# Kernel tuning notes

Measured on AMD Instinct MI355X. Metric: run time of the kernel, lower is better.

Reference implementation:

```python
import jax, jax.numpy as jnp
import numpy as np

NUM_EXPERTS = 8
TOP_K = 2

def setup_inputs() -> dict:
    key = jax.random.key(0)
    ks = jax.random.split(key, 5)
    B, S, D, F, E = 4, 2048, 1024, 4096, NUM_EXPERTS
    x = jax.random.normal(ks[0], (B, S, D), dtype=jnp.float32)
    router_w = jax.random.normal(ks[1], (D, E), dtype=jnp.float32) * 0.02
    router_b = jnp.zeros((E,), dtype=jnp.float32)
    w1 = jax.random.normal(ks[2], (E, D, F), dtype=jnp.float32) * 0.02
    b1 = jnp.zeros((E, F), dtype=jnp.float32)
    w2 = jax.random.normal(ks[3], (E, F, D), dtype=jnp.float32) * 0.02
    b2 = jnp.zeros((E, D), dtype=jnp.float32)
    return {"x": x, "router_w": router_w, "router_b": router_b,
            "w1": w1, "b1": b1, "w2": w2, "b2": b2}

def reference(x, router_w, router_b, w1, b1, w2, b2):
    B, S, D = x.shape
    E = router_w.shape[1]
    x_flat = x.reshape(-1, D)                                  # [N, D]
    router_probs = jax.nn.softmax(x_flat @ router_w + router_b, axis=-1)  # [N, E]
    topk_probs, topk_idx = jax.lax.top_k(router_probs, TOP_K)  # [N, K]
    topk_probs = topk_probs / jnp.sum(topk_probs, axis=-1, keepdims=True)
    # combine weight per (token, expert): sum over top-k slots assigned to that expert
    cw = jnp.sum(topk_probs[..., None] * jax.nn.one_hot(topk_idx, E, dtype=x.dtype), axis=1)  # [N, E]
    out = jnp.zeros_like(x_flat)
    for e in range(E):  # small fixed expert count; each iter is a dense GEMM pair
        h = jax.nn.gelu(x_flat @ w1[e] + b1[e], approximate=False)  # [N, F]
        out = out + cw[:, e:e + 1] * (h @ w2[e] + b2[e])            # [N, D]
    return out.reshape(B, S, D)
```

## Files before the change

### kernel.cpp

```cpp
#include <hip/hip_runtime.h>
#include <hip/hip_bf16.h>

typedef __attribute__((ext_vector_type(8))) __bf16 bf16x8;
typedef __attribute__((ext_vector_type(4))) float f32x4;

#define NTOK 8192
#define D_DIM 1024
#define F_DIM 4096
#define NEXP 8
#define SLOT_TOT 16384
#define SLOT_CAP 16512

__device__ __forceinline__ unsigned short f2b(float f) {
  __hip_bfloat16 b = __float2bfloat16(f);
  return reinterpret_cast<unsigned short&>(b);
}

__device__ __forceinline__ void gload_lds16(const void* g, void* l) {
  __builtin_amdgcn_global_load_lds(
      (__attribute__((address_space(1))) void*)g,
      (__attribute__((address_space(3))) void*)l, 16, 0, 0);
}


__global__ void init_counts_kernel(int* counts) {
  if (threadIdx.x < NEXP) counts[threadIdx.x] = 0;
}

__global__ void zero_out_kernel(float* out) {
  const int i = blockIdx.x * 256 + threadIdx.x;
  reinterpret_cast<float4*>(out)[i] = make_float4(0.f, 0.f, 0.f, 0.f);
}

__global__ void convert_x_kernel(const float* __restrict__ x,
                                 __hip_bfloat16* __restrict__ xb) {
  const int i = (blockIdx.x * 256 + threadIdx.x) * 4;
  const float4 v = *reinterpret_cast<const float4*>(x + i);
  union { unsigned short u[4]; uint2 d; } o;
  o.u[0] = f2b(v.x); o.u[1] = f2b(v.y); o.u[2] = f2b(v.z); o.u[3] = f2b(v.w);
  *reinterpret_cast<uint2*>(xb + i) = o.d;
}

__global__ void transpose_conv_kernel(const float* __restrict__ src,
                                      __hip_bfloat16* __restrict__ dst,
                                      int R, int C) {
  __shared__ float tile[32][33];
  const int e = blockIdx.z;
  src += (size_t)e * R * C;
  dst += (size_t)e * R * C;
  const int c0 = blockIdx.x * 32, r0 = blockIdx.y * 32;
  const int tx = threadIdx.x, ty = threadIdx.y;
  #pragma unroll
  for (int j = 0; j < 32; j += 8)
    tile[ty + j][tx] = src[(size_t)(r0 + ty + j) * C + c0 + tx];
  __syncthreads();
  #pragma unroll
  for (int j = 0; j < 32; j += 8)
    dst[(size_t)(c0 + ty + j) * R + r0 + tx] = __float2bfloat16(tile[tx][ty + j]);
}

__global__ void router_kernel(const float* __restrict__ x,
                              const float* __restrict__ rw,
                              const float* __restrict__ rb,
                              int* __restrict__ topk_idx,
                              float* __restrict__ topk_w,
                              int* __restrict__ counts) {
  __shared__ float rwT[NEXP * D_DIM];
  const int tid = threadIdx.x;
  for (int i = tid; i < NEXP * D_DIM; i += 256) {
    const int d = i >> 3, e = i & 7;
    rwT[e * D_DIM + d] = rw[i];
  }
  __syncthreads();

  const int wave = tid >> 6, lane = tid & 63;
  const int tok = blockIdx.x * 4 + wave;
  const float* xr = x + (size_t)tok * D_DIM;

  float acc[NEXP];
  #pragma unroll
  for (int e = 0; e < NEXP; ++e) acc[e] = 0.f;

  for (int i = 0; i < D_DIM / 64; ++i) {
    const int d = i * 64 + lane;
    const float xv = xr[d];
    #pragma unroll
    for (int e = 0; e < NEXP; ++e) acc[e] += xv * rwT[e * D_DIM + d];
  }
  #pragma unroll
  for (int off = 32; off > 0; off >>= 1) {
    #pragma unroll
    for (int e = 0; e < NEXP; ++e) acc[e] += __shfl_xor(acc[e], off);
  }

  if (lane == 0) {
    float l[NEXP];
    #pragma unroll
    for (int e = 0; e < NEXP; ++e) l[e] = acc[e] + rb[e];
    int i1 = 0;
    #pragma unroll
    for (int e = 1; e < NEXP; ++e) if (l[e] > l[i1]) i1 = e;
    int i2 = (i1 == 0) ? 1 : 0;
    #pragma unroll
    for (int e = 0; e < NEXP; ++e) if (e != i1 && e != i2 && l[e] > l[i2]) i2 = e;
    const float w1 = 1.f / (1.f + __expf(l[i2] - l[i1]));
    topk_idx[tok * 2 + 0] = i1;
    topk_idx[tok * 2 + 1] = i2;
    topk_w[tok * 2 + 0] = w1;
    topk_w[tok * 2 + 1] = 1.f - w1;
    atomicAdd(&counts[i1], 1);
    atomicAdd(&counts[i2], 1);
  }
}

__global__ void offsets_kernel(const int* __restrict__ counts,
                               int* __restrict__ offsets,
                               int* __restrict__ cursors,
                               int* __restrict__ slot_token,
                               float* __restrict__ slot_cw) {
  const int t = threadIdx.x;
  if (t == 0) {
    int s = 0;
    for (int e = 0; e < NEXP; ++e) { offsets[e] = s; cursors[e] = s; s += counts[e]; }
    offsets[NEXP] = s;
  }
  if (t < SLOT_CAP - SLOT_TOT) {
    slot_token[SLOT_TOT + t] = 0;
    slot_cw[SLOT_TOT + t] = 0.f;
  }
}

__global__ void scatter_kernel(const int* __restrict__ topk_idx,
                               const float* __restrict__ topk_w,
                               int* __restrict__ cursors,
                               int* __restrict__ slot_token,
                               float* __restrict__ slot_cw) {
  const int tok = blockIdx.x * 256 + threadIdx.x;
  if (tok >= NTOK) return;
  #pragma unroll
  for (int k = 0; k < 2; ++k) {
    const int e = topk_idx[tok * 2 + k];
    const int p = atomicAdd(&cursors[e], 1);
    slot_token[p] = tok;
    slot_cw[p] = topk_w[tok * 2 + k];
  }
}

template <int PHASE>
__global__ __launch_bounds__(256, 2) void moe_gemm(
    const __hip_bfloat16* __restrict__ A,
    const __hip_bfloat16* __restrict__ B,
    const float* __restrict__ bias,
    const int* __restrict__ slot_token,
    const float* __restrict__ slot_cw,
    const int* __restrict__ counts,
    const int* __restrict__ offsets,
    __hip_bfloat16* __restrict__ Hout,
    float* __restrict__ Out) {
  constexpr int K = (PHASE == 1) ? D_DIM : F_DIM;
  constexpr int NCOL = (PHASE == 1) ? F_DIM : D_DIM;

  const int e = blockIdx.z;
  const int cnt = counts[e];
  const int mt = blockIdx.y;
  if (mt * 128 >= cnt) return;
  const int nt = blockIdx.x;
  const int base = offsets[e];

  __shared__ unsigned short lA[4096];
  __shared__ unsigned short lB[4096];

  const int tid = threadIdx.x;
  const int w = tid >> 6, lane = tid & 63;
  const int r = lane & 15, kg = lane >> 4;
  const int wm = w >> 1, wn = w & 1;

  const int rowA0 = mt * 128 + w * 16 + r;
  const int rowA1 = mt * 128 + (4 + w) * 16 + r;
  const __hip_bfloat16 *gA0, *gA1;
  if constexpr (PHASE == 1) {
    gA0 = A + (size_t)slot_token[base + rowA0] * K + kg * 8;
    gA1 = A + (size_t)slot_token[base + rowA1] * K + kg * 8;
  } else {
    gA0 = A + (size_t)(base + rowA0) * K + kg * 8;
    gA1 = A + (size_t)(base + rowA1) * K + kg * 8;
  }
  const __hip_bfloat16* Be = B + (size_t)e * NCOL * K;
  const __hip_bfloat16* gB0 = Be + (size_t)(nt * 128 + w * 16 + r) * K + kg * 8;
  const __hip_bfloat16* gB1 = Be + (size_t)(nt * 128 + (4 + w) * 16 + r) * K + kg * 8;

  unsigned short* lA0 = &lA[w * 512];
  unsigned short* lA1 = &lA[(4 + w) * 512];
  unsigned short* lB0 = &lB[w * 512];
  unsigned short* lB1 = &lB[(4 + w) * 512];

  f32x4 acc[4][4] = {};

  for (int kt = 0; kt < K / 32; ++kt) {
    gload_lds16(gA0, lA0);
    gload_lds16(gA1, lA1);
    gload_lds16(gB0, lB0);
    gload_lds16(gB1, lB1);
    gA0 += 32; gA1 += 32; gB0 += 32; gB1 += 32;
    __syncthreads();

    bf16x8 af[4], bfr[4];
    #pragma unroll
    for (int i = 0; i < 4; ++i) {
      af[i]  = *(const bf16x8*)&lA[(wm * 4 + i) * 512 + lane * 8];
      bfr[i] = *(const bf16x8*)&lB[(wn * 4 + i) * 512 + lane * 8];
    }
    #pragma unroll
    for (int mi = 0; mi < 4; ++mi)
      #pragma unroll
      for (int ni = 0; ni < 4; ++ni)
        acc[mi][ni] = __builtin_amdgcn_mfma_f32_16x16x32_bf16(af[mi], bfr[ni], acc[mi][ni], 0, 0, 0);
    __syncthreads();
  }

  const int rem = cnt - mt * 128;
  const int q4 = (lane >> 4) * 4;

  if constexpr (PHASE == 1) {
    #pragma unroll
    for (int ni = 0; ni < 4; ++ni) {
      const int col = nt * 128 + wn * 64 + ni * 16 + (lane & 15);
      const float bv = bias[e * NCOL + col];
      #pragma unroll
      for (int mi = 0; mi < 4; ++mi) {
        #pragma unroll
        for (int rr = 0; rr < 4; ++rr) {
          const int rloc = wm * 64 + mi * 16 + q4 + rr;
          if (rloc < rem) {
            float v = acc[mi][ni][rr] + bv;
            v = 0.5f * v * (1.f + erff(v * 0.70710678118654752f));
            Hout[(size_t)(base + mt * 128 + rloc) * F_DIM + col] = __float2bfloat16(v);
          }
        }
      }
    }
  } else {
    #pragma unroll
    for (int mi = 0; mi < 4; ++mi) {
      int toks[4]; float cws[4];
      #pragma unroll
      for (int rr = 0; rr < 4; ++rr) {
        const int rloc = wm * 64 + mi * 16 + q4 + rr;
        const int slot = base + mt * 128 + rloc;
        const bool ok = (rloc < rem);
        toks[rr] = ok ? slot_token[slot] : -1;
        cws[rr]  = ok ? slot_cw[slot] : 0.f;
      }
      #pragma unroll
      for (int ni = 0; ni < 4; ++ni) {
        const int col = nt * 128 + wn * 64 + ni * 16 + (lane & 15);
        const float bv = bias[e * NCOL + col];
        #pragma unroll
        for (int rr = 0; rr < 4; ++rr) {
          if (toks[rr] >= 0)
            atomicAdd(&Out[(size_t)toks[rr] * D_DIM + col], cws[rr] * (acc[mi][ni][rr] + bv));
        }
      }
    }
  }
}


extern "C" void kernel_launch(void* const* d_in, const int* in_sizes, int n_in,
                              void* d_out, int out_size, void* d_ws, size_t ws_size,
                              hipStream_t stream) {
  const float* x  = (const float*)d_in[0];
  const float* rw = (const float*)d_in[1];
  const float* rb = (const float*)d_in[2];
  const float* w1 = (const float*)d_in[3];
  const float* b1 = (const float*)d_in[4];
  const float* w2 = (const float*)d_in[5];
  const float* b2 = (const float*)d_in[6];
  float* out = (float*)d_out;

  char* p = (char*)d_ws;
  size_t used = 0;
  auto carve = [&](size_t bytes) {
    char* r = p + used;
    used += (bytes + 255) & ~(size_t)255;
    return (void*)r;
  };
  __hip_bfloat16* xb  = (__hip_bfloat16*)carve((size_t)NTOK * D_DIM * 2);
  __hip_bfloat16* w1t = (__hip_bfloat16*)carve((size_t)NEXP * F_DIM * D_DIM * 2);
  __hip_bfloat16* w2t = (__hip_bfloat16*)carve((size_t)NEXP * D_DIM * F_DIM * 2);
  __hip_bfloat16* h   = (__hip_bfloat16*)carve((size_t)SLOT_CAP * F_DIM * 2);
  int*   topk_idx   = (int*)carve((size_t)NTOK * 2 * 4);
  float* topk_w     = (float*)carve((size_t)NTOK * 2 * 4);
  int*   slot_token = (int*)carve((size_t)SLOT_CAP * 4);
  float* slot_cw    = (float*)carve((size_t)SLOT_CAP * 4);
  int* counts  = (int*)carve(256);
  int* offsets = (int*)carve(256);
  int* cursors = (int*)carve(256);

  zero_out_kernel<<<8192, 256, 0, stream>>>(out);
  if (used > ws_size) return;

  init_counts_kernel<<<1, 64, 0, stream>>>(counts);
  router_kernel<<<NTOK / 4, 256, 0, stream>>>(x, rw, rb, topk_idx, topk_w, counts);
  offsets_kernel<<<1, 256, 0, stream>>>(counts, offsets, cursors, slot_token, slot_cw);
  scatter_kernel<<<NTOK / 256, 256, 0, stream>>>(topk_idx, topk_w, cursors, slot_token, slot_cw);

  convert_x_kernel<<<(NTOK * D_DIM) / (256 * 4), 256, 0, stream>>>(x, xb);
  dim3 tb(32, 8);
  transpose_conv_kernel<<<dim3(F_DIM / 32, D_DIM / 32, NEXP), tb, 0, stream>>>(w1, w1t, D_DIM, F_DIM);
  transpose_conv_kernel<<<dim3(D_DIM / 32, F_DIM / 32, NEXP), tb, 0, stream>>>(w2, w2t, F_DIM, D_DIM);

  moe_gemm<1><<<dim3(F_DIM / 128, 64, NEXP), 256, 0, stream>>>(
      xb, w1t, b1, slot_token, slot_cw, counts, offsets, h, nullptr);
  moe_gemm<2><<<dim3(D_DIM / 128, 64, NEXP), 256, 0, stream>>>(
      h, w2t, b2, slot_token, slot_cw, counts, offsets, nullptr, out);
}
```

Measured before the change: 1.086 ms.

## Double-buffer LDS in MoE GEMM and vectorize weight transpose-convert

The GEMM main loop now uses two LDS buffers, issuing the next K-tile's global-to-LDS loads before computing on the current one, with one barrier per iteration instead of two. Launch bounds are raised to request four blocks per SM. The weight transpose-convert kernel switches to 64x64 tiles with float4 loads and 4-wide bf16 stores to cut memory transactions. The cost is double the LDS footprint and possible register pressure under the higher occupancy target.

Measured after the change: 1.106 ms. About the same (+1.8%).

```diff
diff --git a/kernel.cpp b/kernel.cpp
--- a/kernel.cpp
+++ b/kernel.cpp
@@ -44,19 +44,30 @@
 __global__ void transpose_conv_kernel(const float* __restrict__ src,
                                       __hip_bfloat16* __restrict__ dst,
                                       int R, int C) {
-  __shared__ float tile[32][33];
+  __shared__ float tile[64][65];
   const int e = blockIdx.z;
   src += (size_t)e * R * C;
   dst += (size_t)e * R * C;
-  const int c0 = blockIdx.x * 32, r0 = blockIdx.y * 32;
+  const int c0 = blockIdx.x * 64, r0 = blockIdx.y * 64;
   const int tx = threadIdx.x, ty = threadIdx.y;
   #pragma unroll
-  for (int j = 0; j < 32; j += 8)
-    tile[ty + j][tx] = src[(size_t)(r0 + ty + j) * C + c0 + tx];
+  for (int j = 0; j < 4; ++j) {
+    const float4 v = *reinterpret_cast<const float4*>(
+        &src[(size_t)(r0 + ty + j * 16) * C + c0 + tx * 4]);
+    tile[ty + j * 16][tx * 4 + 0] = v.x;
+    tile[ty + j * 16][tx * 4 + 1] = v.y;
+    tile[ty + j * 16][tx * 4 + 2] = v.z;
+    tile[ty + j * 16][tx * 4 + 3] = v.w;
+  }
   __syncthreads();
   #pragma unroll
-  for (int j = 0; j < 32; j += 8)
-    dst[(size_t)(c0 + ty + j) * R + r0 + tx] = __float2bfloat16(tile[tx][ty + j]);
+  for (int j = 0; j < 4; ++j) {
+    const int c = ty + j * 16;
+    union { unsigned short u[4]; uint2 d; } o;
+    #pragma unroll
+    for (int i = 0; i < 4; ++i) o.u[i] = f2b(tile[tx * 4 + i][c]);
+    *reinterpret_cast<uint2*>(&dst[(size_t)(c0 + c) * R + r0 + tx * 4]) = o.d;
+  }
 }
 
 __global__ void router_kernel(const float* __restrict__ x,
@@ -147,7 +158,7 @@
 }
 
 template <int PHASE>
-__global__ __launch_bounds__(256, 2) void moe_gemm(
+__global__ __launch_bounds__(256, 4) void moe_gemm(
     const __hip_bfloat16* __restrict__ A,
     const __hip_bfloat16* __restrict__ B,
     const float* __restrict__ bias,
@@ -159,6 +170,7 @@
     float* __restrict__ Out) {
   constexpr int K = (PHASE == 1) ? D_DIM : F_DIM;
   constexpr int NCOL = (PHASE == 1) ? F_DIM : D_DIM;
+  constexpr int KT = K / 32;
 
   const int e = blockIdx.z;
   const int cnt = counts[e];
@@ -167,8 +179,8 @@
   const int nt = blockIdx.x;
   const int base = offsets[e];
 
-  __shared__ unsigned short lA[4096];
-  __shared__ unsigned short lB[4096];
+  __shared__ unsigned short lA[2][4096];
+  __shared__ unsigned short lB[2][4096];
 
   const int tid = threadIdx.x;
   const int w = tid >> 6, lane = tid & 63;
@@ -189,34 +201,39 @@
   const __hip_bfloat16* gB0 = Be + (size_t)(nt * 128 + w * 16 + r) * K + kg * 8;
   const __hip_bfloat16* gB1 = Be + (size_t)(nt * 128 + (4 + w) * 16 + r) * K + kg * 8;
 
-  unsigned short* lA0 = &lA[w * 512];
-  unsigned short* lA1 = &lA[(4 + w) * 512];
-  unsigned short* lB0 = &lB[w * 512];
-  unsigned short* lB1 = &lB[(4 + w) * 512];
-
   f32x4 acc[4][4] = {};
 
-  for (int kt = 0; kt < K / 32; ++kt) {
-    gload_lds16(gA0, lA0);
-    gload_lds16(gA1, lA1);
-    gload_lds16(gB0, lB0);
-    gload_lds16(gB1, lB1);
-    gA0 += 32; gA1 += 32; gB0 += 32; gB1 += 32;
+#define STAGE(b) do {                       \
+    gload_lds16(gA0, &lA[b][w * 512]);      \
+    gload_lds16(gA1, &lA[b][(4 + w) * 512]);\
+    gload_lds16(gB0, &lB[b][w * 512]);      \
+    gload_lds16(gB1, &lB[b][(4 + w) * 512]);\
+    gA0 += 32; gA1 += 32; gB0 += 32; gB1 += 32; } while (0)
+
+#define COMPUTE(b) do {                                                     \
+    bf16x8 af[4], bfr[4];                                                   \
+    _Pragma("unroll") for (int i = 0; i < 4; ++i) {                         \
+      af[i]  = *(const bf16x8*)&lA[b][(wm * 4 + i) * 512 + lane * 8];       \
+      bfr[i] = *(const bf16x8*)&lB[b][(wn * 4 + i) * 512 + lane * 8];       \
+    }                                                                       \
+    _Pragma("unroll") for (int mi = 0; mi < 4; ++mi)                        \
+      _Pragma("unroll") for (int ni = 0; ni < 4; ++ni)                      \
+        acc[mi][ni] = __builtin_amdgcn_mfma_f32_16x16x32_bf16(             \
+            af[mi], bfr[ni], acc[mi][ni], 0, 0, 0); } while (0)
+
+  STAGE(0);
+  __syncthreads();
+  int cur = 0;
+  for (int kt = 0; kt < KT - 1; ++kt) {
+    STAGE(cur ^ 1);
+    COMPUTE(cur);
     __syncthreads();
-
-    bf16x8 af[4], bfr[4];
-    #pragma unroll
-    for (int i = 0; i < 4; ++i) {
-      af[i]  = *(const bf16x8*)&lA[(wm * 4 + i) * 512 + lane * 8];
-      bfr[i] = *(const bf16x8*)&lB[(wn * 4 + i) * 512 + lane * 8];
-    }
-    #pragma unroll
-    for (int mi = 0; mi < 4; ++mi)
-      #pragma unroll
-      for (int ni = 0; ni < 4; ++ni)
-        acc[mi][ni] = __builtin_amdgcn_mfma_f32_16x16x32_bf16(af[mi], bfr[ni], acc[mi][ni], 0, 0, 0);
-    __syncthreads();
-  }
+    cur ^= 1;
+  }
+  COMPUTE(cur);
+
+#undef STAGE
+#undef COMPUTE
 
   const int rem = cnt - mt * 128;
   const int q4 = (lane >> 4) * 4;
@@ -306,9 +323,9 @@
   scatter_kernel<<<NTOK / 256, 256, 0, stream>>>(topk_idx, topk_w, cursors, slot_token, slot_cw);
 
   convert_x_kernel<<<(NTOK * D_DIM) / (256 * 4), 256, 0, stream>>>(x, xb);
-  dim3 tb(32, 8);
-  transpose_conv_kernel<<<dim3(F_DIM / 32, D_DIM / 32, NEXP), tb, 0, stream>>>(w1, w1t, D_DIM, F_DIM);
-  transpose_conv_kernel<<<dim3(D_DIM / 32, F_DIM / 32, NEXP), tb, 0, stream>>>(w2, w2t, F_DIM, D_DIM);
+  dim3 tb(16, 16);
+  transpose_conv_kernel<<<dim3(F_DIM / 64, D_DIM / 64, NEXP), tb, 0, stream>>>(w1, w1t, D_DIM, F_DIM);
+  transpose_conv_kernel<<<dim3(D_DIM / 64, F_DIM / 64, NEXP), tb, 0, stream>>>(w2, w2t, F_DIM, D_DIM);
 
   moe_gemm<1><<<dim3(F_DIM / 128, 64, NEXP), 256, 0, stream>>>(
       xb, w1t, b1, slot_token, slot_cw, counts, offsets, h, nullptr);
```
